# Performance work log

Hardware: AMD Instinct MI355X
Metric: run time of the kernel (lower is better)

The kernel has to match this reference:

```python
import jax, jax.numpy as jnp
import numpy as np

N, E, L, D, H = 20000, 100000, 4, 64, 8
HID = H * D  # LSTM hidden size = num_heads * out_dim


def setup_inputs() -> dict:
    key = jax.random.key(0)
    ks = jax.random.split(key, 8)
    s = 0.05
    return {
        "features": jax.random.normal(ks[0], (N, D), jnp.float32),
        "type_mask": jax.random.randint(ks[1], (N,), 0, 3),
        "edge_metapath_indices": jax.random.randint(ks[2], (E, L), 0, N),
        "dst": jax.random.randint(ks[3], (E,), 0, N),
        "W_ih": jax.random.normal(ks[4], (4 * HID, D), jnp.float32) * s,
        "W_hh": jax.random.normal(ks[5], (4 * HID, HID), jnp.float32) * s,
        "b_ih": jnp.zeros((4 * HID,), jnp.float32),
        "b_hh": jnp.zeros((4 * HID,), jnp.float32),
        "attn1_w": jax.random.normal(ks[6], (H, D), jnp.float32) * s,
        "attn2": jax.random.normal(ks[7], (1, H, D), jnp.float32) * s,
    }


def _lstm_last_hidden(x, W_ih, W_hh, b_ih, b_hh):
    # x: [L, E, D] time-major. PyTorch LSTM gate order: i, f, g, o.
    h0 = jnp.zeros((x.shape[1], W_hh.shape[1]), x.dtype)
    b = b_ih + b_hh

    def step(carry, xt):
        h, c = carry
        gates = xt @ W_ih.T + h @ W_hh.T + b  # [E, 4*HID]
        i, f, g, o = jnp.split(gates, 4, axis=-1)
        c = jax.nn.sigmoid(f) * c + jax.nn.sigmoid(i) * jnp.tanh(g)
        h = jax.nn.sigmoid(o) * jnp.tanh(c)
        return (h, c), None

    (h, _), _ = jax.lax.scan(step, (h0, h0), x)
    return h  # [E, HID]


def reference(features, type_mask, edge_metapath_indices, dst,
              W_ih, W_hh, b_ih, b_hh, attn1_w, attn2):
    alpha = 0.01  # LeakyReLU slope
    # gather metapath node features: [E, L, D]
    edata = features[edge_metapath_indices]
    h = _lstm_last_hidden(jnp.swapaxes(edata, 0, 1), W_ih, W_hh, b_ih, b_hh)
    eft = h.reshape(-1, H, D)  # [E, H, D]
    center = features[edge_metapath_indices[:, -1]]  # [E, D]
    a1 = center @ attn1_w.T                      # [E, H]
    a2 = jnp.sum(eft * attn2, axis=-1)           # [E, H]
    a = jax.nn.leaky_relu(a1 + a2, negative_slope=alpha)[:, :, None]  # [E, H, 1]
    # edge softmax: segmented by destination node
    amax = jax.ops.segment_max(a, dst, num_segments=N)
    amax = jnp.where(jnp.isfinite(amax), amax, 0.0)
    ex = jnp.exp(a - amax[dst])
    denom = jax.ops.segment_sum(ex, dst, num_segments=N)
    attn = ex / denom[dst]  # every edge's segment is nonempty
    # message passing: scatter-sum of eft * attn into dst nodes
    return jax.ops.segment_sum(eft * attn, dst, num_segments=N)  # [N, H, D]
```

## Files before the change

kernel.cpp:

```cpp
#include <hip/hip_runtime.h>
#include <hip/hip_bf16.h>
#include <stdint.h>

#define N_NODES 20000
#define E_EDGES 100000
#define L_SEQ   4
#define D_FEAT  64
#define H_HEADS 8
#define HID     512

typedef __attribute__((ext_vector_type(8))) short short8;
typedef __attribute__((ext_vector_type(4))) float floatx4;

__device__ __forceinline__ float sigmoidf_(float x) { return 1.0f / (1.0f + __expf(-x)); }
__device__ __forceinline__ float tanhf_(float x) {
    x = fminf(15.f, fmaxf(-15.f, x));
    float e = __expf(2.f * x);
    return (e - 1.f) / (e + 1.f);
}
__device__ __forceinline__ unsigned fkey(float f) {
    unsigned u = __float_as_uint(f);
    return (u & 0x80000000u) ? ~u : (u | 0x80000000u);
}
__device__ __forceinline__ float fdecode(unsigned k) {
    if (k == 0u) return 0.0f;
    unsigned u = (k & 0x80000000u) ? (k ^ 0x80000000u) : ~k;
    return __uint_as_float(u);
}
__device__ __forceinline__ short f2bf(float x) {
    __hip_bfloat16 b = __float2bfloat16(x);
    return *(short*)&b;
}
__device__ __forceinline__ float bf2f(short x) {
    __hip_bfloat16 b = *(__hip_bfloat16*)&x;
    return __bfloat162float(b);
}
__device__ __forceinline__ float bfu_lo(unsigned v) { return __uint_as_float((v & 0xffffu) << 16); }
__device__ __forceinline__ float bfu_hi(unsigned v) { return __uint_as_float(v & 0xffff0000u); }

__device__ __forceinline__ void gload16(const void* g, const void* l) {
    __builtin_amdgcn_global_load_lds(
        (const __attribute__((address_space(1))) unsigned int*)(uintptr_t)g,
        (__attribute__((address_space(3))) unsigned int*)(unsigned int)(uintptr_t)l,
        16, 0, 0);
}

__global__ __launch_bounds__(256) void feat2bf16(const float* __restrict__ f, short* __restrict__ fb) {
    int i = blockIdx.x * 256 + threadIdx.x;
    if (i < N_NODES * D_FEAT) fb[i] = f2bf(f[i]);
}

__global__ __launch_bounds__(128) void convert_weights(
    const float* __restrict__ W_ih, const float* __restrict__ W_hh,
    const float* __restrict__ b_ih, const float* __restrict__ b_hh,
    short* __restrict__ Wb_ih, short* __restrict__ Wb_hh, float* __restrict__ bias)
{
    int rp = blockIdx.x;
    int hblock = rp >> 7, rem = rp & 127;
    int half = (rem >> 6) & 1, gate = (rem >> 4) & 3, j = rem & 15;
    int ro = gate * HID + hblock * 32 + half * 16 + j;
    for (int k = threadIdx.x; k < D_FEAT; k += 128)
        Wb_ih[rp * D_FEAT + k] = f2bf(W_ih[ro * D_FEAT + k]);
    for (int k = threadIdx.x; k < HID; k += 128)
        Wb_hh[rp * HID + k] = f2bf(W_hh[ro * HID + k]);
    if (threadIdx.x == 0) bias[ro] = b_ih[ro] + b_hh[ro];
}

__global__ __launch_bounds__(256) void deg_hist(const int* __restrict__ dst, int* __restrict__ deg) {
    int i = blockIdx.x * 256 + threadIdx.x;
    if (i < E_EDGES) atomicAdd(&deg[dst[i]], 1);
}

__global__ __launch_bounds__(1024) void scan_deg(const int* __restrict__ deg,
                                                 int* __restrict__ row, int* __restrict__ cursor) {
    __shared__ int buf[1024];
    __shared__ int s_carry;
    const int tid = threadIdx.x;
    if (tid == 0) s_carry = 0;
    __syncthreads();
    for (int base = 0; base < N_NODES; base += 1024) {
        int idx = base + tid;
        int v = (idx < N_NODES) ? deg[idx] : 0;
        buf[tid] = v;
        __syncthreads();
        for (int offd = 1; offd < 1024; offd <<= 1) {
            int tv = (tid >= offd) ? buf[tid - offd] : 0;
            __syncthreads();
            buf[tid] += tv;
            __syncthreads();
        }
        int c0 = s_carry;
        if (idx < N_NODES) { row[idx] = c0 + buf[tid] - v; cursor[idx] = c0 + buf[tid] - v; }
        __syncthreads();
        if (tid == 1023) s_carry = c0 + buf[1023];
        __syncthreads();
    }
    if (tid == 0) row[N_NODES] = s_carry;
}

__global__ __launch_bounds__(256) void fill_csr(const int* __restrict__ dst,
                                                int* __restrict__ cursor, int* __restrict__ elist) {
    int i = blockIdx.x * 256 + threadIdx.x;
    if (i < E_EDGES) {
        int p = atomicAdd(&cursor[dst[i]], 1);
        elist[p] = i;
    }
}

template <int MODE>
__global__ __launch_bounds__(256) void lstm_mfma(
    const short* __restrict__ feats_bf,
    const int*   __restrict__ mp,
    const short* __restrict__ Wb_ih,
    const short* __restrict__ Wb_hh,
    const float* __restrict__ bias,
    const short* __restrict__ h_src,
    const short* __restrict__ c_src,
    short*       __restrict__ h_dst,
    short*       __restrict__ c_dst,
    int t, int cnt, int nslices)
{
    __shared__ __align__(16) short At[128 * 64];
    __shared__ __align__(16) short Bt[128 * 64];

    const int b     = blockIdx.x;
    const int xcd   = b & 7;
    const int slot  = b >> 3;
    const int g     = slot >> 4;
    const int bn    = slot & 15;
    const int slice = g * 8 + xcd;
    if (slice >= nslices) return;
    const int e0    = slice * 128;
    const int hb    = bn * 32;

    const int tid   = threadIdx.x;
    const int lane  = tid & 63;
    const int w     = tid >> 6;
    const int waveM = w & 1;
    const int waveN = w >> 1;
    const int quad  = lane >> 4;
    const int c16   = lane & 15;

    floatx4 acc[4][4];
#pragma unroll
    for (int a = 0; a < 4; ++a)
#pragma unroll
        for (int bb = 0; bb < 4; ++bb) acc[a][bb] = (floatx4){0.f, 0.f, 0.f, 0.f};

    int eidx[4], mm[4], pgo[4], hrow[4];
#pragma unroll
    for (int i = 0; i < 4; ++i) {
        int s = w * 256 + i * 64 + lane;
        int m = s >> 3, p = s & 7;
        pgo[i] = p ^ (m & 7);
        mm[i]  = m;
        int e  = e0 + m; if (e >= cnt) e = cnt - 1;
        eidx[i] = e;
        if (MODE == 1) hrow[i] = mp[e * L_SEQ];
    }

    const int nch = (MODE == 0) ? 1 : 9;
    for (int kc = 0; kc < nch; ++kc) {
#pragma unroll
        for (int i = 0; i < 4; ++i) {
            int sb = w * 256 + i * 64;
            const void* ga;
            if (kc == 0) {
                int rowf = (MODE == 0) ? eidx[i] : mp[eidx[i] * L_SEQ + t];
                ga = (const void*)(feats_bf + rowf * D_FEAT + pgo[i] * 8);
            } else if (MODE == 1) {
                ga = (const void*)(h_src + (size_t)hrow[i] * HID + (kc - 1) * 64 + pgo[i] * 8);
            } else {
                ga = (const void*)(h_src + (size_t)eidx[i] * HID + (kc - 1) * 64 + pgo[i] * 8);
            }
            gload16(ga, (const void*)&At[sb * 8]);
            int r = bn * 128 + mm[i];
            const void* gb = (kc == 0)
                ? (const void*)(Wb_ih + r * D_FEAT + pgo[i] * 8)
                : (const void*)(Wb_hh + (size_t)r * HID + (kc - 1) * 64 + pgo[i] * 8);
            gload16(gb, (const void*)&Bt[sb * 8]);
        }
        __syncthreads();

#pragma unroll
        for (int ks = 0; ks < 2; ++ks) {
            short8 af[4], bfv[4];
#pragma unroll
            for (int mf = 0; mf < 4; ++mf) {
                int m  = waveM * 64 + mf * 16 + c16;
                int pw = ks * 4 + quad;
                af[mf] = *(const short8*)&At[m * 64 + ((pw ^ (m & 7)) * 8)];
            }
#pragma unroll
            for (int nf = 0; nf < 4; ++nf) {
                int n  = waveN * 64 + nf * 16 + c16;
                int pw = ks * 4 + quad;
                bfv[nf] = *(const short8*)&Bt[n * 64 + ((pw ^ (n & 7)) * 8)];
            }
#pragma unroll
            for (int mf = 0; mf < 4; ++mf)
#pragma unroll
                for (int nf = 0; nf < 4; ++nf)
                    acc[mf][nf] = __builtin_amdgcn_mfma_f32_16x16x32_bf16(
                        af[mf], bfv[nf], acc[mf][nf], 0, 0, 0);
        }
        __syncthreads();
    }

    const int n = hb + waveN * 16 + c16;
    const float bi  = bias[n];
    const float bff = bias[HID + n];
    const float bg  = bias[2 * HID + n];
    const float bo  = bias[3 * HID + n];
#pragma unroll
    for (int mf = 0; mf < 4; ++mf) {
#pragma unroll
        for (int r = 0; r < 4; ++r) {
            int e = e0 + waveM * 64 + mf * 16 + quad * 4 + r;
            if (e < cnt) {
                float gi = acc[mf][0][r] + bi;
                float gf = acc[mf][1][r] + bff;
                float gg = acc[mf][2][r] + bg;
                float go = acc[mf][3][r] + bo;
                float c_old;
                if (MODE == 0)      c_old = 0.f;
                else if (MODE == 1) c_old = bf2f(c_src[(size_t)mp[e * L_SEQ] * HID + n]);
                else                c_old = bf2f(c_src[(size_t)e * HID + n]);
                float cn = sigmoidf_(gf) * c_old + sigmoidf_(gi) * tanhf_(gg);
                if (MODE != 3) c_dst[(size_t)e * HID + n] = f2bf(cn);
                h_dst[(size_t)e * HID + n] = f2bf(sigmoidf_(go) * tanhf_(cn));
            }
        }
    }
}

__global__ __launch_bounds__(256) void attn_logits(
    const float* __restrict__ features,
    const int*   __restrict__ mp,
    const short* __restrict__ hfin,
    const float* __restrict__ attn1_w,
    const float* __restrict__ attn2,
    float*       __restrict__ a_out)
{
    const int e    = blockIdx.x * 4 + (threadIdx.x >> 6);
    const int lane = threadIdx.x & 63;
    const int ctr  = mp[e * L_SEQ + (L_SEQ - 1)];
#pragma unroll
    for (int p = 0; p < 2; ++p) {
        const int h  = p * 4 + (lane >> 4);
        const int d4 = (lane & 15) * 4;
        const float4 cd = *(const float4*)&features[ctr * D_FEAT + d4];
        const float4 a1 = *(const float4*)&attn1_w[h * D_FEAT + d4];
        const float4 a2 = *(const float4*)&attn2[h * D_FEAT + d4];
        const uint2 ev = *(const uint2*)&hfin[(size_t)e * HID + h * D_FEAT + d4];
        float v = cd.x * a1.x + cd.y * a1.y + cd.z * a1.z + cd.w * a1.w
                + bfu_lo(ev.x) * a2.x + bfu_hi(ev.x) * a2.y
                + bfu_lo(ev.y) * a2.z + bfu_hi(ev.y) * a2.w;
#pragma unroll
        for (int off = 1; off < 16; off <<= 1) v += __shfl_xor(v, off, 64);
        if ((lane & 15) == 0) {
            float lv = v > 0.f ? v : 0.01f * v;
            a_out[e * H_HEADS + h] = lv;
        }
    }
}

__global__ __launch_bounds__(256) void gather_out(
    const int*   __restrict__ row,
    const int*   __restrict__ elist,
    const float* __restrict__ a_scr,
    const short* __restrict__ eft,
    float*       __restrict__ out)
{
    const int n   = blockIdx.x;
    const int tid = threadIdx.x;
    const int beg = row[n];
    const int deg = row[n + 1] - beg;
    const int j   = tid * 2;
    const int h   = tid >> 5;

    if (deg == 0) {
        *(float2*)&out[(size_t)n * HID + j] = (float2){0.f, 0.f};
        return;
    }

    __shared__ unsigned s_maxu[H_HEADS];
    __shared__ float    s_max[H_HEADS];
    __shared__ float    s_den[H_HEADS];
    __shared__ float    s_w[128 * H_HEADS];
    __shared__ int      s_e[128];

    if (tid < H_HEADS) { s_maxu[tid] = 0u; s_den[tid] = 0.f; }
    __syncthreads();
    for (int i = tid; i < deg * H_HEADS; i += 256) {
        int e = elist[beg + (i >> 3)], hh = i & 7;
        atomicMax(&s_maxu[hh], fkey(a_scr[e * H_HEADS + hh]));
    }
    __syncthreads();
    if (tid < H_HEADS) s_max[tid] = fdecode(s_maxu[tid]);
    __syncthreads();
    for (int i = tid; i < deg * H_HEADS; i += 256) {
        int e = elist[beg + (i >> 3)], hh = i & 7;
        atomicAdd(&s_den[hh], __expf(a_scr[e * H_HEADS + hh] - s_max[hh]));
    }
    __syncthreads();

    float acc0 = 0.f, acc1 = 0.f;
    for (int c0 = 0; c0 < deg; c0 += 128) {
        int cc = min(128, deg - c0);
        if (tid < cc) s_e[tid] = elist[beg + c0 + tid];
        __syncthreads();
        for (int i = tid; i < cc * H_HEADS; i += 256) {
            int k = i >> 3, hh = i & 7;
            s_w[k * H_HEADS + hh] = __expf(a_scr[s_e[k] * H_HEADS + hh] - s_max[hh]) / s_den[hh];
        }
        __syncthreads();
        for (int k = 0; k < cc; ++k) {
            unsigned v = *(const unsigned*)&eft[(size_t)s_e[k] * HID + j];
            float wgt = s_w[k * H_HEADS + h];
            acc0 += wgt * bfu_lo(v);
            acc1 += wgt * bfu_hi(v);
        }
        __syncthreads();
    }
    *(float2*)&out[(size_t)n * HID + j] = (float2){acc0, acc1};
}

extern "C" void kernel_launch(void* const* d_in, const int* in_sizes, int n_in,
                              void* d_out, int out_size, void* d_ws, size_t ws_size,
                              hipStream_t stream) {
    const float* features = (const float*)d_in[0];
    const int*   mp       = (const int*)d_in[2];
    const int*   dst      = (const int*)d_in[3];
    const float* W_ih     = (const float*)d_in[4];
    const float* W_hh     = (const float*)d_in[5];
    const float* b_ih     = (const float*)d_in[6];
    const float* b_hh     = (const float*)d_in[7];
    const float* attn1_w  = (const float*)d_in[8];
    const float* attn2    = (const float*)d_in[9];
    float* out = (float*)d_out;

    char* ws = (char*)d_ws;
    size_t off = 0;
    float* a_scr    = (float*)(ws + off); off += (size_t)E_EDGES * H_HEADS * sizeof(float);
    int*   deg      = (int*)(ws + off);   off += (size_t)N_NODES * sizeof(int);
    int*   row      = (int*)(ws + off);   off += ((size_t)N_NODES + 1) * sizeof(int);
    int*   cursor   = (int*)(ws + off);   off += (size_t)N_NODES * sizeof(int);
    int*   elist    = (int*)(ws + off);   off += (size_t)E_EDGES * sizeof(int);
    short* feats_bf = (short*)(ws + off); off += (size_t)N_NODES * D_FEAT * sizeof(short);
    short* Wb_ih    = (short*)(ws + off); off += (size_t)4 * HID * D_FEAT * sizeof(short);
    short* Wb_hh    = (short*)(ws + off); off += (size_t)4 * HID * HID * sizeof(short);
    float* bias     = (float*)(ws + off); off += (size_t)4 * HID * sizeof(float);
    off = (off + 255) & ~(size_t)255;
    short* h1n      = (short*)(ws + off); off += (size_t)N_NODES * HID * sizeof(short);
    short* c1n      = (short*)(ws + off); off += (size_t)N_NODES * HID * sizeof(short);
    off = (off + 255) & ~(size_t)255;
    short* eft      = (short*)(ws + off); off += (size_t)E_EDGES * HID * sizeof(short);
    off = (off + 255) & ~(size_t)255;

    const size_t per_edge = (size_t)HID * (2 + 2 + 2);
    size_t avail = (ws_size > off) ? (ws_size - off) : 0;
    long long cs_ll = ((long long)(avail / per_edge) / 1024) * 1024;
    int cs = (int)(cs_ll < 1024 ? 1024 : (cs_ll > E_EDGES ? E_EDGES : cs_ll));

    short* hA = (short*)(ws + off);
    short* hB = hA + (size_t)cs * HID;
    short* cS = hB + (size_t)cs * HID;

    hipMemsetAsync(deg, 0, (size_t)N_NODES * sizeof(int), stream);
    deg_hist<<<(E_EDGES + 255) / 256, 256, 0, stream>>>(dst, deg);
    scan_deg<<<1, 1024, 0, stream>>>(deg, row, cursor);
    fill_csr<<<(E_EDGES + 255) / 256, 256, 0, stream>>>(dst, cursor, elist);

    feat2bf16<<<(N_NODES * D_FEAT + 255) / 256, 256, 0, stream>>>(features, feats_bf);
    convert_weights<<<4 * HID, 128, 0, stream>>>(W_ih, W_hh, b_ih, b_hh, Wb_ih, Wb_hh, bias);

    {
        int nslices = (N_NODES + 127) / 128;
        int nblk = ((nslices + 7) & ~7) * 16;
        lstm_mfma<0><<<nblk, 256, 0, stream>>>(feats_bf, nullptr, Wb_ih, Wb_hh, bias,
                                               nullptr, nullptr, h1n, c1n, 0, N_NODES, nslices);
    }

    for (int e0 = 0; e0 < E_EDGES; e0 += cs) {
        int cnt = E_EDGES - e0 < cs ? E_EDGES - e0 : cs;
        int nslices = (cnt + 127) / 128;
        int nblk = ((nslices + 7) & ~7) * 16;
        const int* mpc = mp + (size_t)e0 * L_SEQ;
        short* eft_c = eft + (size_t)e0 * HID;
        lstm_mfma<1><<<nblk, 256, 0, stream>>>(feats_bf, mpc, Wb_ih, Wb_hh, bias, h1n, c1n, hA, cS, 1, cnt, nslices);
        lstm_mfma<2><<<nblk, 256, 0, stream>>>(feats_bf, mpc, Wb_ih, Wb_hh, bias, hA, cS, hB, cS, 2, cnt, nslices);
        lstm_mfma<3><<<nblk, 256, 0, stream>>>(feats_bf, mpc, Wb_ih, Wb_hh, bias, hB, cS, eft_c, nullptr, 3, cnt, nslices);
    }

    attn_logits<<<E_EDGES / 4, 256, 0, stream>>>(features, mp, eft, attn1_w, attn2, a_scr);
    gather_out<<<N_NODES, 256, 0, stream>>>(row, elist, a_scr, eft, out);
}
```

Before: 1.345 ms.

## Switch LSTM GEMM to 32x32x16 MFMA with two-wave 128-thread blocks

Recasts the LSTM gate GEMM kernel to use 32x32x16 bf16 MFMA tiles instead of 16x16x32, with each of two waves covering 64 rows by all 128 gate columns. The weight row permutation is changed so each gate's 32 hidden units are contiguous, matching the new accumulator layout. Gather offsets are precomputed once per thread instead of reloading metapath indices every K chunk. Blocks shrink to 128 threads with launch bounds asking for two blocks per SIMD group. The aim is fewer LDS fragment reads per MFMA and less index overhead, at the cost of more accumulator registers per thread.

```diff
diff --git a/kernel.cpp b/kernel.cpp
--- a/kernel.cpp
+++ b/kernel.cpp
@@ -9,8 +9,8 @@
 #define H_HEADS 8
 #define HID     512
 
-typedef __attribute__((ext_vector_type(8))) short short8;
-typedef __attribute__((ext_vector_type(4))) float floatx4;
+typedef __attribute__((ext_vector_type(8)))  short short8;
+typedef __attribute__((ext_vector_type(16))) float floatx16;
 
 __device__ __forceinline__ float sigmoidf_(float x) { return 1.0f / (1.0f + __expf(-x)); }
 __device__ __forceinline__ float tanhf_(float x) {
@@ -57,8 +57,8 @@
 {
     int rp = blockIdx.x;
     int hblock = rp >> 7, rem = rp & 127;
-    int half = (rem >> 6) & 1, gate = (rem >> 4) & 3, j = rem & 15;
-    int ro = gate * HID + hblock * 32 + half * 16 + j;
+    int gate = rem >> 5, hu = rem & 31;
+    int ro = gate * HID + hblock * 32 + hu;
     for (int k = threadIdx.x; k < D_FEAT; k += 128)
         Wb_ih[rp * D_FEAT + k] = f2bf(W_ih[ro * D_FEAT + k]);
     for (int k = threadIdx.x; k < HID; k += 128)
@@ -108,7 +108,7 @@
 }
 
 template <int MODE>
-__global__ __launch_bounds__(256) void lstm_mfma(
+__global__ __launch_bounds__(128, 2) void lstm_mfma(
     const short* __restrict__ feats_bf,
     const int*   __restrict__ mp,
     const short* __restrict__ Wb_ih,
@@ -136,87 +136,82 @@
     const int tid   = threadIdx.x;
     const int lane  = tid & 63;
     const int w     = tid >> 6;
-    const int waveM = w & 1;
-    const int waveN = w >> 1;
-    const int quad  = lane >> 4;
-    const int c16   = lane & 15;
-
-    floatx4 acc[4][4];
-#pragma unroll
-    for (int a = 0; a < 4; ++a)
-#pragma unroll
-        for (int bb = 0; bb < 4; ++bb) acc[a][bb] = (floatx4){0.f, 0.f, 0.f, 0.f};
-
-    int eidx[4], mm[4], pgo[4], hrow[4];
-#pragma unroll
-    for (int i = 0; i < 4; ++i) {
-        int s = w * 256 + i * 64 + lane;
+    const int l31   = lane & 31;
+    const int khalf = lane >> 5;
+
+    floatx16 acc[2][4];
+#pragma unroll
+    for (int mf = 0; mf < 2; ++mf)
+#pragma unroll
+        for (int nf = 0; nf < 4; ++nf)
+#pragma unroll
+            for (int r = 0; r < 16; ++r) acc[mf][nf][r] = 0.f;
+
+    int a0off[8], b0off[8], aoff[8], boff[8];
+#pragma unroll
+    for (int i = 0; i < 8; ++i) {
+        int s = w * 512 + i * 64 + lane;
         int m = s >> 3, p = s & 7;
-        pgo[i] = p ^ (m & 7);
-        mm[i]  = m;
-        int e  = e0 + m; if (e >= cnt) e = cnt - 1;
-        eidx[i] = e;
-        if (MODE == 1) hrow[i] = mp[e * L_SEQ];
+        int pg = p ^ (m & 7);
+        int e = e0 + m; if (e >= cnt) e = cnt - 1;
+        int rowf = (MODE == 0) ? e : mp[e * L_SEQ + t];
+        a0off[i] = rowf * D_FEAT + pg * 8;
+        b0off[i] = (bn * 128 + m) * D_FEAT + pg * 8;
+        if (MODE != 0) {
+            int hr = (MODE == 1) ? mp[e * L_SEQ] : e;
+            aoff[i] = hr * HID + pg * 8;
+            boff[i] = (bn * 128 + m) * HID + pg * 8;
+        }
     }
 
     const int nch = (MODE == 0) ? 1 : 9;
     for (int kc = 0; kc < nch; ++kc) {
-#pragma unroll
-        for (int i = 0; i < 4; ++i) {
-            int sb = w * 256 + i * 64;
-            const void* ga;
-            if (kc == 0) {
-                int rowf = (MODE == 0) ? eidx[i] : mp[eidx[i] * L_SEQ + t];
-                ga = (const void*)(feats_bf + rowf * D_FEAT + pgo[i] * 8);
-            } else if (MODE == 1) {
-                ga = (const void*)(h_src + (size_t)hrow[i] * HID + (kc - 1) * 64 + pgo[i] * 8);
-            } else {
-                ga = (const void*)(h_src + (size_t)eidx[i] * HID + (kc - 1) * 64 + pgo[i] * 8);
+        const int ko = (kc - 1) * 64;
+#pragma unroll
+        for (int i = 0; i < 8; ++i) {
+            int sb = w * 512 + i * 64;
+            const short* ga = (kc == 0) ? (feats_bf + a0off[i]) : (h_src + aoff[i] + ko);
+            const short* gb = (kc == 0) ? (Wb_ih + b0off[i])    : (Wb_hh + boff[i] + ko);
+            gload16((const void*)ga, (const void*)&At[sb * 8]);
+            gload16((const void*)gb, (const void*)&Bt[sb * 8]);
+        }
+        __syncthreads();
+
+#pragma unroll
+        for (int ks = 0; ks < 4; ++ks) {
+            const int kx = ks * 2 + khalf;
+            short8 af[2], bfv[4];
+#pragma unroll
+            for (int mf = 0; mf < 2; ++mf) {
+                int m = w * 64 + mf * 32 + l31;
+                af[mf] = *(const short8*)&At[m * 64 + ((kx ^ (m & 7)) * 8)];
             }
-            gload16(ga, (const void*)&At[sb * 8]);
-            int r = bn * 128 + mm[i];
-            const void* gb = (kc == 0)
-                ? (const void*)(Wb_ih + r * D_FEAT + pgo[i] * 8)
-                : (const void*)(Wb_hh + (size_t)r * HID + (kc - 1) * 64 + pgo[i] * 8);
-            gload16(gb, (const void*)&Bt[sb * 8]);
-        }
-        __syncthreads();
-
-#pragma unroll
-        for (int ks = 0; ks < 2; ++ks) {
-            short8 af[4], bfv[4];
-#pragma unroll
-            for (int mf = 0; mf < 4; ++mf) {
-                int m  = waveM * 64 + mf * 16 + c16;
-                int pw = ks * 4 + quad;
-                af[mf] = *(const short8*)&At[m * 64 + ((pw ^ (m & 7)) * 8)];
+#pragma unroll
+            for (int nf = 0; nf < 4; ++nf) {
+                int n = nf * 32 + l31;
+                bfv[nf] = *(const short8*)&Bt[n * 64 + ((kx ^ (n & 7)) * 8)];
             }
 #pragma unroll
-            for (int nf = 0; nf < 4; ++nf) {
-                int n  = waveN * 64 + nf * 16 + c16;
-                int pw = ks * 4 + quad;
-                bfv[nf] = *(const short8*)&Bt[n * 64 + ((pw ^ (n & 7)) * 8)];
-            }
-#pragma unroll
-            for (int mf = 0; mf < 4; ++mf)
+            for (int mf = 0; mf < 2; ++mf)
 #pragma unroll
                 for (int nf = 0; nf < 4; ++nf)
-                    acc[mf][nf] = __builtin_amdgcn_mfma_f32_16x16x32_bf16(
+                    acc[mf][nf] = __builtin_amdgcn_mfma_f32_32x32x16_bf16(
                         af[mf], bfv[nf], acc[mf][nf], 0, 0, 0);
         }
         __syncthreads();
     }
 
-    const int n = hb + waveN * 16 + c16;
+    const int n = hb + l31;
     const float bi  = bias[n];
     const float bff = bias[HID + n];
     const float bg  = bias[2 * HID + n];
     const float bo  = bias[3 * HID + n];
 #pragma unroll
-    for (int mf = 0; mf < 4; ++mf) {
-#pragma unroll
-        for (int r = 0; r < 4; ++r) {
-            int e = e0 + waveM * 64 + mf * 16 + quad * 4 + r;
+    for (int mf = 0; mf < 2; ++mf) {
+#pragma unroll
+        for (int r = 0; r < 16; ++r) {
+            int rowm = (r & 3) + 8 * (r >> 2) + 4 * khalf;
+            int e = e0 + w * 64 + mf * 32 + rowm;
             if (e < cnt) {
                 float gi = acc[mf][0][r] + bi;
                 float gf = acc[mf][1][r] + bff;
@@ -378,7 +373,7 @@
     {
         int nslices = (N_NODES + 127) / 128;
         int nblk = ((nslices + 7) & ~7) * 16;
-        lstm_mfma<0><<<nblk, 256, 0, stream>>>(feats_bf, nullptr, Wb_ih, Wb_hh, bias,
+        lstm_mfma<0><<<nblk, 128, 0, stream>>>(feats_bf, nullptr, Wb_ih, Wb_hh, bias,
                                                nullptr, nullptr, h1n, c1n, 0, N_NODES, nslices);
     }
 
@@ -388,9 +383,9 @@
         int nblk = ((nslices + 7) & ~7) * 16;
         const int* mpc = mp + (size_t)e0 * L_SEQ;
         short* eft_c = eft + (size_t)e0 * HID;
-        lstm_mfma<1><<<nblk, 256, 0, stream>>>(feats_bf, mpc, Wb_ih, Wb_hh, bias, h1n, c1n, hA, cS, 1, cnt, nslices);
-        lstm_mfma<2><<<nblk, 256, 0, stream>>>(feats_bf, mpc, Wb_ih, Wb_hh, bias, hA, cS, hB, cS, 2, cnt, nslices);
-        lstm_mfma<3><<<nblk, 256, 0, stream>>>(feats_bf, mpc, Wb_ih, Wb_hh, bias, hB, cS, eft_c, nullptr, 3, cnt, nslices);
+        lstm_mfma<1><<<nblk, 128, 0, stream>>>(feats_bf, mpc, Wb_ih, Wb_hh, bias, h1n, c1n, hA, cS, 1, cnt, nslices);
+        lstm_mfma<2><<<nblk, 128, 0, stream>>>(feats_bf, mpc, Wb_ih, Wb_hh, bias, hA, cS, hB, cS, 2, cnt, nslices);
+        lstm_mfma<3><<<nblk, 128, 0, stream>>>(feats_bf, mpc, Wb_ih, Wb_hh, bias, hB, cS, eft_c, nullptr, 3, cnt, nslices);
     }
 
     attn_logits<<<E_EDGES / 4, 256, 0, stream>>>(features, mp, eft, attn1_w, attn2, a_scr);
```

Measured after the change: 1.595 ms. +18.6%, slower.
